# Kernel tuning notes

Measured on AMD Instinct MI355X. Metric: run time of the kernel, lower is better.

## Reference

```python
import jax, jax.numpy as jnp
import numpy as np

# Dims: B nodes, Z species (elements), IN/OUT channels, M = 2*l+1 (l=1)
B, Z, IN, OUT, M = 8192, 10, 512, 512, 3
ALPHA = 1.0 / np.sqrt(IN)  # self.alpha = 1/sqrt(in_dim)
SQRT3 = float(np.sqrt(3.0))


def setup_inputs() -> dict:
    key = jax.random.key(0)
    k1, k2, k3 = jax.random.split(key, 3)
    t = jax.random.normal(k1, (B, IN, M), dtype=jnp.float32)
    species = jax.random.randint(k2, (B,), 0, Z)
    node_attrs = jax.nn.one_hot(species, Z, dtype=jnp.float32)  # [B, Z] one-hot
    # torch.nn.init.uniform_(weights, -sqrt(3), sqrt(3))
    weights = jax.random.uniform(k3, (Z, OUT, IN), dtype=jnp.float32,
                                 minval=-SQRT3, maxval=SQRT3)
    return {"t": t, "node_attrs": node_attrs, "weights": weights}


def reference(t, node_attrs, weights):
    # Faithful to: einsum('bz, zCc, bcd -> bCd', node_attrs, weights*alpha, t)
    # Contract weights with t first per species ([Z,B,C,M], ~500MB), which
    # avoids the huge [B,C,c] per-node weight-gather intermediate, then
    # select/sum over species with the one-hot node_attrs.
    W = weights * ALPHA                       # [Z, OUT, IN]
    zt = jnp.einsum('zCc,bcd->zbCd', W, t)    # [Z, B, OUT, M]
    out = jnp.einsum('bz,zbCd->bCd', node_attrs, zt)  # [B, OUT, M]
    return out
```

## Files before the change

### kernel.cpp

```cpp
#include <hip/hip_runtime.h>
#include <stdint.h>

#define NB   8192
#define NZ   10
#define CIN  512
#define COUT 512
#define MM   3
#define ALPHA 0.04419417382415922f

#define ROWS_TOTAL (NB * MM)
#define BM 128
#define BN 128
#define BK 32
#define KITERS (CIN / BK)
#define MAX_MT (ROWS_TOTAL / BM + NZ)

typedef short bf16x8 __attribute__((ext_vector_type(8)));
typedef float f32x4  __attribute__((ext_vector_type(4)));

__device__ __forceinline__ uint16_t f2bf(float f) {
    union { float f; uint32_t i; } v; v.f = f;
    uint32_t x = v.i;
    x += 0x7fffu + ((x >> 16) & 1u);
    return (uint16_t)(x >> 16);
}
__device__ __forceinline__ uint32_t pack2(float a, float b) {
    return (uint32_t)f2bf(a) | ((uint32_t)f2bf(b) << 16);
}
__device__ __forceinline__ void async16(const ushort* g, ushort* l) {
    __builtin_amdgcn_global_load_lds((const uint32_t*)g, (uint32_t*)l, 16, 0, 0);
}

__global__ __launch_bounds__(256)
void decode_count(const float* __restrict__ attrs, int* __restrict__ species,
                  int* __restrict__ cnt) {
    const int b = blockIdx.x * 256 + threadIdx.x;
    const float* a = attrs + (size_t)b * NZ;
    int s = 0;
    #pragma unroll
    for (int z = 0; z < NZ; z++) if (a[z] > 0.5f) s = z;
    species[b] = s;
    const int lane = threadIdx.x & 63;
    #pragma unroll
    for (int z = 0; z < NZ; z++) {
        unsigned long long m = __ballot(s == z);
        if (lane == 0 && m) atomicAdd(&cnt[z], __popcll(m));
    }
}

__global__ void scan_kernel(const int* __restrict__ cnt, int* __restrict__ offsets,
                            int* __restrict__ tile_offsets, int* __restrict__ cur) {
    if (threadIdx.x == 0) {
        int off = 0, toff = 0;
        for (int z = 0; z < NZ; z++) {
            offsets[z] = off; tile_offsets[z] = toff; cur[z] = off;
            off  += cnt[z];
            toff += (3 * cnt[z] + BM - 1) / BM;
        }
        offsets[NZ] = off; tile_offsets[NZ] = toff;
    }
}

__global__ __launch_bounds__(256)
void place_kernel(const int* __restrict__ species, int* __restrict__ cur,
                  int* __restrict__ sorted) {
    const int b = blockIdx.x * 256 + threadIdx.x;
    const int s = species[b];
    const int lane = threadIdx.x & 63;
    #pragma unroll
    for (int z = 0; z < NZ; z++) {
        unsigned long long m = __ballot(s == z);
        if (s == z) {
            int leader = __ffsll((unsigned long long)m) - 1;
            int rank = __popcll(m & ((1ull << lane) - 1ull));
            int base = 0;
            if (lane == leader) base = atomicAdd(&cur[z], __popcll(m));
            base = __shfl(base, leader);
            sorted[base + rank] = b;
        }
    }
}

__global__ __launch_bounds__(256)
void pack_t(const float* __restrict__ t, const int* __restrict__ sorted,
            ushort* __restrict__ tt) {
    const int w = threadIdx.x >> 6, L = threadIdx.x & 63;
    const int p = blockIdx.x * 4 + w;
    const int node = sorted[p];
    const float4* src = (const float4*)(t + (size_t)node * (CIN * MM) + L * 24);
    float4 f[6];
    #pragma unroll
    for (int i = 0; i < 6; i++) f[i] = src[i];
    const float* v = (const float*)f;
    #pragma unroll
    for (int d = 0; d < MM; d++) {
        uint4 o;
        o.x = pack2(v[d],      v[3 + d]);
        o.y = pack2(v[6 + d],  v[9 + d]);
        o.z = pack2(v[12 + d], v[15 + d]);
        o.w = pack2(v[18 + d], v[21 + d]);
        *(uint4*)&tt[(size_t)(3 * p + d) * CIN + L * 8] = o;
    }
}

__global__ __launch_bounds__(256)
void pack_w(const float* __restrict__ w, ushort* __restrict__ wt) {
    const int i = (blockIdx.x * 256 + threadIdx.x) * 8;
    float4 a = *(const float4*)(w + i);
    float4 b = *(const float4*)(w + i + 4);
    uint4 o;
    o.x = pack2(a.x, a.y); o.y = pack2(a.z, a.w);
    o.z = pack2(b.x, b.y); o.w = pack2(b.z, b.w);
    *(uint4*)(wt + i) = o;
}

__global__ __launch_bounds__(256)
void gemm_kernel(const ushort* __restrict__ tt, const ushort* __restrict__ wt,
                 const int* __restrict__ sorted, const int* __restrict__ offsets,
                 const int* __restrict__ tile_offsets, float* __restrict__ out) {
    __shared__ ushort As[BM][BK];
    __shared__ ushort Bs[BN][BK];

    const int tz = blockIdx.x;
    if (tz >= tile_offsets[NZ]) return;
    int z = 0;
    #pragma unroll
    for (int i = 1; i < NZ; i++) if (tile_offsets[i] <= tz) z = i;

    const int row_base = 3 * offsets[z] + (tz - tile_offsets[z]) * BM;
    const int row_end  = 3 * offsets[z + 1];
    const int Cbase    = blockIdx.y * BN;

    const int tid = threadIdx.x;
    const int w = tid >> 6, L = tid & 63;

    const int lrow = L >> 2;
    const int lk   = (L & 3) * 8;
    const ushort* gA = tt + (size_t)(row_base + w * 32 + lrow) * CIN + lk;
    const ushort* gB = wt + ((size_t)z * COUT + Cbase + w * 32 + lrow) * CIN + lk;
    ushort* lA0 = &As[w * 32][0];
    ushort* lA1 = &As[w * 32 + 16][0];
    ushort* lB0 = &Bs[w * 32][0];
    ushort* lB1 = &Bs[w * 32 + 16][0];

    const int wm = w & 1, wn = w >> 1;
    const int q = L >> 4, mr = L & 15;

    f32x4 acc[4][4];
    #pragma unroll
    for (int i = 0; i < 4; i++)
        #pragma unroll
        for (int j = 0; j < 4; j++) acc[i][j] = (f32x4){0.f, 0.f, 0.f, 0.f};

    for (int kt = 0; kt < KITERS; kt++) {
        const int ko = kt * BK;
        async16(gA + ko, lA0);
        async16(gA + (size_t)16 * CIN + ko, lA1);
        async16(gB + ko, lB0);
        async16(gB + (size_t)16 * CIN + ko, lB1);
        __syncthreads();

        bf16x8 af[4], bf[4];
        #pragma unroll
        for (int am = 0; am < 4; am++)
            af[am] = *(const bf16x8*)&As[wm * 64 + am * 16 + mr][q * 8];
        #pragma unroll
        for (int bn = 0; bn < 4; bn++)
            bf[bn] = *(const bf16x8*)&Bs[wn * 64 + bn * 16 + mr][q * 8];
        #pragma unroll
        for (int am = 0; am < 4; am++)
            #pragma unroll
            for (int bn = 0; bn < 4; bn++)
                acc[am][bn] = __builtin_amdgcn_mfma_f32_16x16x32_bf16(
                    af[am], bf[bn], acc[am][bn], 0, 0, 0);
        __syncthreads();
    }

    #pragma unroll
    for (int am = 0; am < 4; am++) {
        #pragma unroll
        for (int r = 0; r < 4; r++) {
            const int Rg = row_base + wm * 64 + am * 16 + q * 4 + r;
            if (Rg < row_end) {
                const int pos = Rg / 3;
                const int d = Rg - 3 * pos;
                const int node = sorted[pos];
                float* o = out + (size_t)node * (COUT * MM) + d;
                #pragma unroll
                for (int bn = 0; bn < 4; bn++) {
                    const int Cg = Cbase + wn * 64 + bn * 16 + mr;
                    o[(size_t)Cg * 3] = ALPHA * acc[am][bn][r];
                }
            }
        }
    }
}

extern "C" void kernel_launch(void* const* d_in, const int* in_sizes, int n_in,
                              void* d_out, int out_size, void* d_ws, size_t ws_size,
                              hipStream_t stream) {
    const float* t     = (const float*)d_in[0];
    const float* attrs = (const float*)d_in[1];
    const float* w     = (const float*)d_in[2];
    float* out = (float*)d_out;

    uint8_t* ws = (uint8_t*)d_ws;
    int* species      = (int*)ws;                        ws += NB * 4;
    int* sorted       = (int*)ws;                        ws += NB * 4;
    int* cnt          = (int*)ws;                        ws += 16 * 4;
    int* offsets      = (int*)ws;                        ws += 16 * 4;
    int* tile_offsets = (int*)ws;                        ws += 16 * 4;
    int* cur          = (int*)ws;                        ws += 16 * 4;
    ws = (uint8_t*)(((uintptr_t)ws + 255) & ~(uintptr_t)255);
    ushort* wt = (ushort*)ws;                            ws += (size_t)NZ * COUT * CIN * 2;
    ushort* tt = (ushort*)ws;

    hipMemsetAsync(cnt, 0, 16 * 4, stream);
    hipLaunchKernelGGL(decode_count, dim3(NB / 256), dim3(256), 0, stream,
                       attrs, species, cnt);
    hipLaunchKernelGGL(scan_kernel, dim3(1), dim3(64), 0, stream,
                       cnt, offsets, tile_offsets, cur);
    hipLaunchKernelGGL(place_kernel, dim3(NB / 256), dim3(256), 0, stream,
                       species, cur, sorted);
    hipLaunchKernelGGL(pack_t, dim3(NB / 4), dim3(256), 0, stream,
                       t, sorted, tt);
    hipLaunchKernelGGL(pack_w, dim3((NZ * COUT * CIN) / (256 * 8)), dim3(256), 0, stream,
                       w, wt);
    hipLaunchKernelGGL(gemm_kernel, dim3(MAX_MT, COUT / BN), dim3(256), 0, stream,
                       tt, wt, sorted, offsets, tile_offsets, out);
}
```

Before: 186.5 us.

## Merge prep kernels, deterministic sort, halve GEMM N-tile, cache node ids in LDS

Fuses species decode, per-block histogram and weight bf16 packing into one launch. It replaces the atomic count/scan/place chain with a deterministic two-kernel histogram-based placement, removing the memset and the single-thread scan launch. The GEMM N-tile drops from 128 to 64, giving twice as many blocks and fewer accumulators but more A re-reads. Epilogue node ids are staged in shared memory instead of being read from global memory.

```diff
diff --git a/kernel.cpp b/kernel.cpp
--- a/kernel.cpp
+++ b/kernel.cpp
@@ -10,10 +10,11 @@
 
 #define ROWS_TOTAL (NB * MM)
 #define BM 128
-#define BN 128
+#define BN 64
 #define BK 32
 #define KITERS (CIN / BK)
 #define MAX_MT (ROWS_TOTAL / BM + NZ)
+#define NGRP 32
 
 typedef short bf16x8 __attribute__((ext_vector_type(8)));
 typedef float f32x4  __attribute__((ext_vector_type(4)));
@@ -32,53 +33,87 @@
 }
 
 __global__ __launch_bounds__(256)
-void decode_count(const float* __restrict__ attrs, int* __restrict__ species,
-                  int* __restrict__ cnt) {
-    const int b = blockIdx.x * 256 + threadIdx.x;
+void prep_kernel(const float* __restrict__ attrs, const float* __restrict__ w,
+                 int* __restrict__ species, int* __restrict__ hist,
+                 ushort* __restrict__ wt) {
+    const int tid = threadIdx.x;
+    if (blockIdx.x >= NGRP) {
+        const size_t i = ((size_t)(blockIdx.x - NGRP) * 256 + tid) * 8;
+        float4 a = *(const float4*)(w + i);
+        float4 b = *(const float4*)(w + i + 4);
+        uint4 o;
+        o.x = pack2(a.x, a.y); o.y = pack2(a.z, a.w);
+        o.z = pack2(b.x, b.y); o.w = pack2(b.z, b.w);
+        *(uint4*)(wt + i) = o;
+        return;
+    }
+    __shared__ int wc[4][NZ];
+    const int b = blockIdx.x * 256 + tid;
     const float* a = attrs + (size_t)b * NZ;
     int s = 0;
     #pragma unroll
     for (int z = 0; z < NZ; z++) if (a[z] > 0.5f) s = z;
     species[b] = s;
-    const int lane = threadIdx.x & 63;
+    const int wv = tid >> 6, lane = tid & 63;
     #pragma unroll
     for (int z = 0; z < NZ; z++) {
         unsigned long long m = __ballot(s == z);
-        if (lane == 0 && m) atomicAdd(&cnt[z], __popcll(m));
-    }
-}
-
-__global__ void scan_kernel(const int* __restrict__ cnt, int* __restrict__ offsets,
-                            int* __restrict__ tile_offsets, int* __restrict__ cur) {
-    if (threadIdx.x == 0) {
+        if (lane == 0) wc[wv][z] = __popcll(m);
+    }
+    __syncthreads();
+    if (tid < NZ) {
+        hist[blockIdx.x * NZ + tid] = wc[0][tid] + wc[1][tid] + wc[2][tid] + wc[3][tid];
+    }
+}
+
+__global__ __launch_bounds__(256)
+void place_kernel(const int* __restrict__ species, const int* __restrict__ hist,
+                  int* __restrict__ sorted, int* __restrict__ offsets,
+                  int* __restrict__ tile_offsets) {
+    __shared__ int lhist[NGRP][NZ];
+    __shared__ int loff[NZ + 1], ltoff[NZ + 1];
+    __shared__ int pb[NZ];
+    __shared__ int wc[4][NZ];
+    const int tid = threadIdx.x, g = blockIdx.x;
+
+    for (int i = tid; i < NGRP * NZ; i += 256) ((int*)lhist)[i] = hist[i];
+    __syncthreads();
+    if (tid == 0) {
         int off = 0, toff = 0;
         for (int z = 0; z < NZ; z++) {
-            offsets[z] = off; tile_offsets[z] = toff; cur[z] = off;
-            off  += cnt[z];
-            toff += (3 * cnt[z] + BM - 1) / BM;
+            int tot = 0;
+            for (int gg = 0; gg < NGRP; gg++) tot += lhist[gg][z];
+            loff[z] = off; ltoff[z] = toff;
+            off += tot;
+            toff += (3 * tot + BM - 1) / BM;
         }
-        offsets[NZ] = off; tile_offsets[NZ] = toff;
-    }
-}
-
-__global__ __launch_bounds__(256)
-void place_kernel(const int* __restrict__ species, int* __restrict__ cur,
-                  int* __restrict__ sorted) {
-    const int b = blockIdx.x * 256 + threadIdx.x;
+        loff[NZ] = off; ltoff[NZ] = toff;
+    }
+    __syncthreads();
+    if (tid < NZ) {
+        int base = loff[tid];
+        for (int gg = 0; gg < g; gg++) base += lhist[gg][tid];
+        pb[tid] = base;
+    }
+    if (g == 0 && tid < NZ + 1) {
+        offsets[tid] = loff[tid];
+        tile_offsets[tid] = ltoff[tid];
+    }
+    const int b = g * 256 + tid;
     const int s = species[b];
-    const int lane = threadIdx.x & 63;
+    const int wv = tid >> 6, lane = tid & 63;
+    unsigned long long mymask = 0;
     #pragma unroll
     for (int z = 0; z < NZ; z++) {
         unsigned long long m = __ballot(s == z);
-        if (s == z) {
-            int leader = __ffsll((unsigned long long)m) - 1;
-            int rank = __popcll(m & ((1ull << lane) - 1ull));
-            int base = 0;
-            if (lane == leader) base = atomicAdd(&cur[z], __popcll(m));
-            base = __shfl(base, leader);
-            sorted[base + rank] = b;
-        }
-    }
+        if (lane == 0) wc[wv][z] = __popcll(m);
+        if (s == z) mymask = m;
+    }
+    __syncthreads();
+    int rank = __popcll(mymask & ((1ull << lane) - 1ull));
+    #pragma unroll
+    for (int w2 = 0; w2 < 4; w2++) if (w2 < wv) rank += wc[w2][s];
+    sorted[pb[s] + rank] = b;
 }
 
 __global__ __launch_bounds__(256)
@@ -104,22 +139,12 @@
 }
 
 __global__ __launch_bounds__(256)
-void pack_w(const float* __restrict__ w, ushort* __restrict__ wt) {
-    const int i = (blockIdx.x * 256 + threadIdx.x) * 8;
-    float4 a = *(const float4*)(w + i);
-    float4 b = *(const float4*)(w + i + 4);
-    uint4 o;
-    o.x = pack2(a.x, a.y); o.y = pack2(a.z, a.w);
-    o.z = pack2(b.x, b.y); o.w = pack2(b.z, b.w);
-    *(uint4*)(wt + i) = o;
-}
-
-__global__ __launch_bounds__(256)
 void gemm_kernel(const ushort* __restrict__ tt, const ushort* __restrict__ wt,
                  const int* __restrict__ sorted, const int* __restrict__ offsets,
                  const int* __restrict__ tile_offsets, float* __restrict__ out) {
     __shared__ ushort As[BM][BK];
     __shared__ ushort Bs[BN][BK];
+    __shared__ int spos[48];
 
     const int tz = blockIdx.x;
     if (tz >= tile_offsets[NZ]) return;
@@ -129,48 +154,49 @@
 
     const int row_base = 3 * offsets[z] + (tz - tile_offsets[z]) * BM;
     const int row_end  = 3 * offsets[z + 1];
+    const int pos0     = row_base / 3;
     const int Cbase    = blockIdx.y * BN;
 
     const int tid = threadIdx.x;
     const int w = tid >> 6, L = tid & 63;
+
+    if (tid < 48) spos[tid] = sorted[min(pos0 + tid, NB - 1)];
 
     const int lrow = L >> 2;
     const int lk   = (L & 3) * 8;
     const ushort* gA = tt + (size_t)(row_base + w * 32 + lrow) * CIN + lk;
-    const ushort* gB = wt + ((size_t)z * COUT + Cbase + w * 32 + lrow) * CIN + lk;
+    const ushort* gB = wt + ((size_t)z * COUT + Cbase + w * 16 + lrow) * CIN + lk;
     ushort* lA0 = &As[w * 32][0];
     ushort* lA1 = &As[w * 32 + 16][0];
-    ushort* lB0 = &Bs[w * 32][0];
-    ushort* lB1 = &Bs[w * 32 + 16][0];
+    ushort* lB0 = &Bs[w * 16][0];
 
     const int wm = w & 1, wn = w >> 1;
     const int q = L >> 4, mr = L & 15;
 
-    f32x4 acc[4][4];
+    f32x4 acc[4][2];
     #pragma unroll
     for (int i = 0; i < 4; i++)
         #pragma unroll
-        for (int j = 0; j < 4; j++) acc[i][j] = (f32x4){0.f, 0.f, 0.f, 0.f};
+        for (int j = 0; j < 2; j++) acc[i][j] = (f32x4){0.f, 0.f, 0.f, 0.f};
 
     for (int kt = 0; kt < KITERS; kt++) {
         const int ko = kt * BK;
         async16(gA + ko, lA0);
         async16(gA + (size_t)16 * CIN + ko, lA1);
         async16(gB + ko, lB0);
-        async16(gB + (size_t)16 * CIN + ko, lB1);
         __syncthreads();
 
-        bf16x8 af[4], bf[4];
+        bf16x8 af[4], bf[2];
         #pragma unroll
         for (int am = 0; am < 4; am++)
             af[am] = *(const bf16x8*)&As[wm * 64 + am * 16 + mr][q * 8];
         #pragma unroll
-        for (int bn = 0; bn < 4; bn++)
-            bf[bn] = *(const bf16x8*)&Bs[wn * 64 + bn * 16 + mr][q * 8];
+        for (int bn = 0; bn < 2; bn++)
+            bf[bn] = *(const bf16x8*)&Bs[wn * 32 + bn * 16 + mr][q * 8];
         #pragma unroll
         for (int am = 0; am < 4; am++)
             #pragma unroll
-            for (int bn = 0; bn < 4; bn++)
+            for (int bn = 0; bn < 2; bn++)
                 acc[am][bn] = __builtin_amdgcn_mfma_f32_16x16x32_bf16(
                     af[am], bf[bn], acc[am][bn], 0, 0, 0);
         __syncthreads();
@@ -184,11 +210,11 @@
             if (Rg < row_end) {
                 const int pos = Rg / 3;
                 const int d = Rg - 3 * pos;
-                const int node = sorted[pos];
+                const int node = spos[pos - pos0];
                 float* o = out + (size_t)node * (COUT * MM) + d;
                 #pragma unroll
-                for (int bn = 0; bn < 4; bn++) {
-                    const int Cg = Cbase + wn * 64 + bn * 16 + mr;
+                for (int bn = 0; bn < 2; bn++) {
+                    const int Cg = Cbase + wn * 32 + bn * 16 + mr;
                     o[(size_t)Cg * 3] = ALPHA * acc[am][bn][r];
                 }
             }
@@ -205,27 +231,20 @@
     float* out = (float*)d_out;
 
     uint8_t* ws = (uint8_t*)d_ws;
-    int* species      = (int*)ws;                        ws += NB * 4;
-    int* sorted       = (int*)ws;                        ws += NB * 4;
-    int* cnt          = (int*)ws;                        ws += 16 * 4;
-    int* offsets      = (int*)ws;                        ws += 16 * 4;
-    int* tile_offsets = (int*)ws;                        ws += 16 * 4;
-    int* cur          = (int*)ws;                        ws += 16 * 4;
+    int* species      = (int*)ws;                  ws += NB * 4;
+    int* sorted       = (int*)ws;                  ws += NB * 4;
+    int* hist         = (int*)ws;                  ws += NGRP * NZ * 4;
+    int* offsets      = (int*)ws;                  ws += 16 * 4;
+    int* tile_offsets = (int*)ws;                  ws += 16 * 4;
     ws = (uint8_t*)(((uintptr_t)ws + 255) & ~(uintptr_t)255);
-    ushort* wt = (ushort*)ws;                            ws += (size_t)NZ * COUT * CIN * 2;
+    ushort* wt = (ushort*)ws;                      ws += (size_t)NZ * COUT * CIN * 2;
     ushort* tt = (ushort*)ws;
 
-    hipMemsetAsync(cnt, 0, 16 * 4, stream);
-    hipLaunchKernelGGL(decode_count, dim3(NB / 256), dim3(256), 0, stream,
-                       attrs, species, cnt);
-    hipLaunchKernelGGL(scan_kernel, dim3(1), dim3(64), 0, stream,
-                       cnt, offsets, tile_offsets, cur);
-    hipLaunchKernelGGL(place_kernel, dim3(NB / 256), dim3(256), 0, stream,
-                       species, cur, sorted);
-    hipLaunchKernelGGL(pack_t, dim3(NB / 4), dim3(256), 0, stream,
-                       t, sorted, tt);
-    hipLaunchKernelGGL(pack_w, dim3((NZ * COUT * CIN) / (256 * 8)), dim3(256), 0, stream,
-                       w, wt);
+    hipLaunchKernelGGL(prep_kernel, dim3(NGRP + (NZ * COUT * CIN) / 2048), dim3(256),
+                       0, stream, attrs, w, species, hist, wt);
+    hipLaunchKernelGGL(place_kernel, dim3(NGRP), dim3(256), 0, stream,
+                       species, hist, sorted, offsets, tile_offsets);
+    hipLaunchKernelGGL(pack_t, dim3(NB / 4), dim3(256), 0, stream, t, sorted, tt);
     hipLaunchKernelGGL(gemm_kernel, dim3(MAX_MT, COUT / BN), dim3(256), 0, stream,
                        tt, wt, sorted, offsets, tile_offsets, out);
 }
```

New measurement: 159.7 us. -14.4%, faster.
